# Kernel tuning notes

Measured on AMD Instinct MI355X. Metric: run time of the kernel, lower is better.

Reference implementation:

```python
import jax, jax.numpy as jnp
import numpy as np

HEADS = 8


def setup_inputs() -> dict:
    key = jax.random.key(0)
    ks = jax.random.split(key, 7)
    b, t, e, h = 4, 2048, 128, HEADS
    x = jax.random.normal(ks[0], (b, t, e), dtype=jnp.float32)
    mask = jax.random.randint(ks[1], (1, t, t), 0, 2, dtype=jnp.int32)
    Wq = jax.random.normal(ks[2], (e, e * h), dtype=jnp.float32) / np.sqrt(e)
    Wk = jax.random.normal(ks[3], (e, e * h), dtype=jnp.float32) / np.sqrt(e)
    Wv = jax.random.normal(ks[4], (e, e * h), dtype=jnp.float32) / np.sqrt(e)
    Wu = jax.random.normal(ks[5], (e * h, e), dtype=jnp.float32) / np.sqrt(e * h)
    bu = jax.random.normal(ks[6], (e,), dtype=jnp.float32) * 0.01
    return {"x": x, "mask": mask, "Wq": Wq, "Wk": Wk, "Wv": Wv, "Wu": Wu, "bu": bu}


def reference(x, mask, Wq, Wk, Wv, Wu, bu):
    b, t, e = x.shape
    h = HEADS
    scale = e ** (-0.25)  # original scales q and k each by e**(1/4)
    # project and split heads: (b, t, h, e) -> (b, h, t, e)
    q = (x @ Wq).reshape(b, t, h, e).transpose(0, 2, 1, 3) * scale
    k = (x @ Wk).reshape(b, t, h, e).transpose(0, 2, 1, 3) * scale
    v = (x @ Wv).reshape(b, t, h, e).transpose(0, 2, 1, 3)
    dot = jnp.einsum('bhqe,bhke->bhqk', q, k)  # (b, h, t, t)
    # causal mask: strictly-upper triangle set to -inf (mask_diagonal=False -> offset=1)
    causal = jnp.triu(jnp.ones((t, t), dtype=bool), k=1)
    dot = jnp.where(causal, jnp.float32(-np.inf), dot)
    # external mask: positions where mask == 0 set to -1e9 (broadcast over b*h)
    dot = jnp.where((mask == 0)[:, None, :, :], jnp.float32(-1e9), dot)
    att = jax.nn.softmax(dot, axis=-1)
    out = jnp.einsum('bhqk,bhke->bhqe', att, v)
    out = out.transpose(0, 2, 1, 3).reshape(b, t, h * e)
    return out @ Wu + bu
```

## Files before the change

kernel.cpp:

```cpp
#include <hip/hip_runtime.h>
#include <hip/hip_bf16.h>

typedef unsigned short u16;
typedef unsigned int u32;
typedef __attribute__((ext_vector_type(8))) short bf16x8;
typedef __attribute__((ext_vector_type(4))) float f32x4;
typedef __attribute__((ext_vector_type(8))) unsigned short u16x8;
typedef __attribute__((ext_vector_type(2))) unsigned int u32x2;

#define T_ 2048
#define H_ 8
#define BH_ 32
#define M_ 8192
#define SCALE_QK 0.29730177875068026f

__device__ __forceinline__ u16 f2bf(float f) {
  union { __hip_bfloat16 h; u16 u; } cv; cv.h = __float2bfloat16(f); return cv.u;
}
__device__ __forceinline__ float bf2f(u16 u) {
  union { u16 u; __hip_bfloat16 h; } cv; cv.u = u; return __bfloat162float(cv.h);
}
__device__ __forceinline__ void gload16(const u16* g, u16* l) {
  __builtin_amdgcn_global_load_lds(
      (const __attribute__((address_space(1))) void*)g,
      (__attribute__((address_space(3))) void*)l, 16, 0, 0);
}


__global__ __launch_bounds__(256)
void prep_kernel(const float* __restrict__ x, const float* __restrict__ Wq,
                 const float* __restrict__ Wk, const float* __restrict__ Wv,
                 const float* __restrict__ Wu,
                 u16* __restrict__ xb, u16* __restrict__ WT, u16* __restrict__ WuT)
{
  int i = blockIdx.x * 256 + threadIdx.x;
  if (i < M_ * 128) { xb[i] = f2bf(x[i]); return; }
  int j = i - M_ * 128;
  if (j < 3072 * 128) {
    int n = j >> 7, k = j & 127;
    float w;
    if (n < 1024)      w = Wq[k * 1024 + n] * SCALE_QK;
    else if (n < 2048) w = Wk[k * 1024 + (n - 1024)] * SCALE_QK;
    else               w = Wv[k * 1024 + (n - 2048)];
    WT[j] = f2bf(w);
    return;
  }
  int u = j - 3072 * 128;
  if (u < 128 * 1024) {
    int n = u >> 10, k = u & 1023;
    WuT[u] = f2bf(Wu[k * 128 + n]);
  }
}

__global__ __launch_bounds__(256)
void maskprep_kernel(const int* __restrict__ mask, u32* __restrict__ mbits,
                     u32* __restrict__ deglist, u32* __restrict__ degcount,
                     float* __restrict__ cnt0inv)
{
  int wave = threadIdx.x >> 6, lane = threadIdx.x & 63;
  int q = blockIdx.x * 4 + wave;
  const int* row = mask + (long)q * 2048;
  unsigned long long anyvis = 0ull;
  int cnt1 = 0;
  for (int it = 0; it < 32; ++it) {
    int k = it * 64 + lane;
    unsigned long long bal = __ballot(row[k] != 0);
    if (lane == 0) {
      mbits[q * 64 + it * 2]     = (u32)bal;
      mbits[q * 64 + it * 2 + 1] = (u32)(bal >> 32);
    }
    cnt1 += __popcll(bal);
    int lim = q - it * 64;
    if (lim >= 63)      anyvis |= bal;
    else if (lim >= 0)  anyvis |= (bal & ((2ull << lim) - 1ull));
  }
  if (lane == 0) {
    int c0 = 2048 - cnt1;
    cnt0inv[q] = (c0 > 0) ? 1.0f / (float)c0 : 0.0f;
    if (anyvis == 0ull) {
      u32 slot = atomicAdd(degcount, 1u);
      deglist[slot] = (u32)q;
    }
  }
}

__global__ __launch_bounds__(256)
void qkv_kernel(const u16* __restrict__ xb, const u16* __restrict__ WT,
                u16* __restrict__ Qb, u16* __restrict__ Kimg, u16* __restrict__ Vimg)
{
  __shared__ __align__(16) u16 As[128 * 128];
  __shared__ __align__(16) u16 Bs[128 * 128];
  const int tid = threadIdx.x;
  const int n0 = blockIdx.x * 128;
  const int m0 = blockIdx.y * 128;
#pragma unroll
  for (int i = 0; i < 8; ++i) {
    int c = tid + 256 * i;
    int row = c >> 4, d0 = (c & 15) * 8;
    int soff = row * 128 + ((((d0 >> 3)) ^ (row & 15)) << 3);
    *(u16x8*)(&As[soff]) = *(const u16x8*)(&xb[(m0 + row) * 128 + d0]);
    *(u16x8*)(&Bs[soff]) = *(const u16x8*)(&WT[(n0 + row) * 128 + d0]);
  }
  __syncthreads();
  const int wave = tid >> 6, lane = tid & 63;
  const int lr = lane & 15, lg = lane >> 4;
  const int wm = (wave >> 1) * 64, wn = (wave & 1) * 64;
  f32x4 acc[4][4];
#pragma unroll
  for (int a = 0; a < 4; ++a)
#pragma unroll
    for (int b = 0; b < 4; ++b) acc[a][b] = (f32x4){0.f, 0.f, 0.f, 0.f};
#pragma unroll
  for (int ks = 0; ks < 4; ++ks) {
    bf16x8 af[4], bf[4];
#pragma unroll
    for (int mt = 0; mt < 4; ++mt) {
      int row = wm + mt * 16 + lr, chunk = lg + ks * 4;
      af[mt] = *(const bf16x8*)(&As[row * 128 + ((chunk ^ (row & 15)) << 3)]);
    }
#pragma unroll
    for (int nt = 0; nt < 4; ++nt) {
      int row = wn + nt * 16 + lr, chunk = lg + ks * 4;
      bf[nt] = *(const bf16x8*)(&Bs[row * 128 + ((chunk ^ (row & 15)) << 3)]);
    }
#pragma unroll
    for (int mt = 0; mt < 4; ++mt)
#pragma unroll
      for (int nt = 0; nt < 4; ++nt)
        acc[mt][nt] = __builtin_amdgcn_mfma_f32_16x16x32_bf16(af[mt], bf[nt], acc[mt][nt], 0, 0, 0);
  }
  const int mat = n0 >> 10;
  const int hh = (n0 & 1023) >> 7;
  const int bb = m0 >> 11;
  const long bhb = (long)(bb * H_ + hh);
  __syncthreads();
  if (mat != 2) {
#pragma unroll
    for (int mt = 0; mt < 4; ++mt)
#pragma unroll
      for (int nt = 0; nt < 4; ++nt)
#pragma unroll
        for (int r = 0; r < 4; ++r) {
          int tl = wm + mt * 16 + lg * 4 + r;
          int d  = wn + nt * 16 + lr;
          As[tl * 128 + ((((d >> 3)) ^ (tl & 15)) << 3) + (d & 7)] = f2bf(acc[mt][nt][r]);
        }
    __syncthreads();
    if (mat == 0) {
#pragma unroll
      for (int i = 0; i < 8; ++i) {
        int c = tid + 256 * i;
        int row = c >> 4, d0 = (c & 15) * 8;
        u16x8 v = *(const u16x8*)(&As[row * 128 + ((((d0 >> 3)) ^ (row & 15)) << 3)]);
        *(u16x8*)(&Qb[(bhb * T_ + ((m0 + row) & 2047)) * 128 + d0]) = v;
      }
    } else {
#pragma unroll
      for (int i = 0; i < 8; ++i) {
        int c = tid + 256 * i;
        int row = c >> 4, d0 = (c & 15) * 8;
        u16x8 v = *(const u16x8*)(&As[row * 128 + ((((d0 >> 3)) ^ (row & 15)) << 3)]);
        int t = (m0 + row) & 2047;
        int kt = t >> 6, kr = t & 63;
        *(u16x8*)(&Kimg[(bhb * 32 + kt) * 8192 + kr * 128 + ((((d0 >> 3)) ^ (kr & 15)) << 3)]) = v;
      }
    }
  } else {
    u16* TT = As;
#pragma unroll
    for (int mt = 0; mt < 4; ++mt)
#pragma unroll
      for (int nt = 0; nt < 4; ++nt)
#pragma unroll
        for (int r = 0; r < 4; ++r) {
          int tl = wm + mt * 16 + lg * 4 + r;
          int d  = wn + nt * 16 + lr;
          TT[d * 128 + ((((tl >> 3)) ^ (d & 15)) << 3) + (tl & 7)] = f2bf(acc[mt][nt][r]);
        }
    __syncthreads();
    const int tg0 = m0 & 2047;
#pragma unroll
    for (int i = 0; i < 8; ++i) {
      int c = tid + 256 * i;
      int d = c >> 4, t0 = (c & 15) * 8;
      u16x8 v = *(const u16x8*)(&TT[d * 128 + ((((t0 >> 3)) ^ (d & 15)) << 3)]);
      int tg = tg0 + t0;
      int kt = tg >> 6, kk = tg & 63;
      *(u16x8*)(&Vimg[(bhb * 32 + kt) * 8192 + d * 64 + (((kk >> 3) ^ (d & 7)) << 3)]) = v;
    }
  }
}

__global__ __launch_bounds__(256, 4)
void flash_kernel(const u16* __restrict__ Qb, const u16* __restrict__ Kimg,
                  const u16* __restrict__ Vimg, const u32* __restrict__ mbits,
                  u16* __restrict__ Ob)
{
  __shared__ __align__(16) u16 Ks[64 * 128];
  __shared__ __align__(16) u16 VTs[128 * 64];
  __shared__ __align__(16) u16 Ps[4][16 * 64];
  const int tid = threadIdx.x;
  const int qt = 31 - (blockIdx.x >> 5);
  const int bh = blockIdx.x & 31;
  const int q0 = qt * 64;
  const int wave = tid >> 6, lane = tid & 63;
  const int lr = lane & 15, lg = lane >> 4;
  const long base = (long)bh * T_ * 128;
  const long iblk = (long)bh * 32;
  const int woff = wave * 2048;
  const int qrl = wave * 16 + lr;
  const int swz = (lr & 7) << 1;

  bf16x8 qf[4];
  {
    const u16* qrow = Qb + base + (long)(q0 + qrl) * 128;
#pragma unroll
    for (int ks = 0; ks < 4; ++ks)
      qf[ks] = *(const bf16x8*)(&qrow[lg * 8 + ks * 32]);
  }
  f32x4 acc[8];
#pragma unroll
  for (int i = 0; i < 8; ++i) acc[i] = (f32x4){0.f, 0.f, 0.f, 0.f};
  float mrun = -__builtin_inff(), lrun = 0.f;

  for (int kt = 0; kt <= qt; ++kt) {
    const int kv0 = kt * 64;
    __syncthreads();
    {
      const u16* ks = Kimg + (iblk + kt) * 8192 + woff + lane * 8;
      const u16* vs = Vimg + (iblk + kt) * 8192 + woff + lane * 8;
#pragma unroll
      for (int i = 0; i < 4; ++i) gload16(ks + i * 512, &Ks[woff + i * 512]);
#pragma unroll
      for (int i = 0; i < 4; ++i) gload16(vs + i * 512, &VTs[woff + i * 512]);
    }
    u32 mw0, mw1;
    {
      const u32* mp = &mbits[(q0 + qrl) * 64 + (kv0 >> 5)];
      mw0 = mp[0]; mw1 = mp[1];
    }
    __syncthreads();

    f32x4 s[4];
    __builtin_amdgcn_s_setprio(1);
#pragma unroll
    for (int ft = 0; ft < 4; ++ft) {
      f32x4 sa = (f32x4){0.f, 0.f, 0.f, 0.f};
#pragma unroll
      for (int ks = 0; ks < 4; ++ks) {
        int kr = ft * 16 + lr, chunk = lg + ks * 4;
        bf16x8 kf = *(const bf16x8*)(&Ks[kr * 128 + ((chunk ^ (kr & 15)) << 3)]);
        sa = __builtin_amdgcn_mfma_f32_16x16x32_bf16(kf, qf[ks], sa, 0, 0, 0);
      }
      s[ft] = sa;
    }
    __builtin_amdgcn_s_setprio(0);
    const bool diag = (kt == qt);
#pragma unroll
    for (int ft = 0; ft < 4; ++ft) {
      u32 w = (ft & 2) ? mw1 : mw0;
      int kbase = ft * 16 + lg * 4;
      int sh = ((ft & 1) << 4) + lg * 4;
#pragma unroll
      for (int r = 0; r < 4; ++r) {
        bool vis = (w >> (sh + r)) & 1u;
        if (diag && (kbase + r) > qrl) vis = false;
        if (!vis) s[ft][r] = -__builtin_inff();
      }
    }
    float t0 = fmaxf(fmaxf(s[0][0], s[0][1]), fmaxf(s[0][2], s[0][3]));
    float t1 = fmaxf(fmaxf(s[1][0], s[1][1]), fmaxf(s[1][2], s[1][3]));
    float t2 = fmaxf(fmaxf(s[2][0], s[2][1]), fmaxf(s[2][2], s[2][3]));
    float t3 = fmaxf(fmaxf(s[3][0], s[3][1]), fmaxf(s[3][2], s[3][3]));
    float tm = fmaxf(fmaxf(t0, t1), fmaxf(t2, t3));
    tm = fmaxf(tm, __shfl_xor(tm, 16));
    tm = fmaxf(tm, __shfl_xor(tm, 32));
    float mnew = fmaxf(mrun, tm);
    float msafe = (mnew == -__builtin_inff()) ? 0.f : mnew;
    float fac = __expf(mrun - msafe);
    mrun = mnew;
    float rs = 0.f;
#pragma unroll
    for (int ft = 0; ft < 4; ++ft) {
      float p0 = __expf(s[ft][0] - msafe), p1 = __expf(s[ft][1] - msafe);
      float p2 = __expf(s[ft][2] - msafe), p3 = __expf(s[ft][3] - msafe);
      s[ft][0] = p0; s[ft][1] = p1; s[ft][2] = p2; s[ft][3] = p3;
      rs += (p0 + p1) + (p2 + p3);
    }
    rs += __shfl_xor(rs, 16);
    rs += __shfl_xor(rs, 32);
    lrun = lrun * fac + rs;
#pragma unroll
    for (int nt = 0; nt < 8; ++nt)
#pragma unroll
      for (int r = 0; r < 4; ++r) acc[nt][r] *= fac;
#pragma unroll
    for (int ft = 0; ft < 4; ++ft) {
      u16 h0 = f2bf(s[ft][0]), h1 = f2bf(s[ft][1]);
      u16 h2 = f2bf(s[ft][2]), h3 = f2bf(s[ft][3]);
      u32x2 pw; pw[0] = (u32)h0 | ((u32)h1 << 16); pw[1] = (u32)h2 | ((u32)h3 << 16);
      int ch4 = (ft * 4 + lg) ^ swz;
      *(u32x2*)(&Ps[wave][lr * 64 + ch4 * 4]) = pw;
    }
    bf16x8 pa[2];
#pragma unroll
    for (int s2 = 0; s2 < 2; ++s2) {
      int ch4b = (s2 * 8 + lg * 2) ^ swz;
      pa[s2] = *(const bf16x8*)(&Ps[wave][lr * 64 + ch4b * 4]);
    }
    __builtin_amdgcn_s_setprio(1);
#pragma unroll
    for (int nt = 0; nt < 8; ++nt)
#pragma unroll
      for (int s2 = 0; s2 < 2; ++s2) {
        int d = nt * 16 + lr, chunk = lg + s2 * 4;
        bf16x8 vf = *(const bf16x8*)(&VTs[d * 64 + ((chunk ^ (d & 7)) << 3)]);
        acc[nt] = __builtin_amdgcn_mfma_f32_16x16x32_bf16(vf, pa[s2], acc[nt], 0, 0, 0);
      }
    __builtin_amdgcn_s_setprio(0);
  }
  const float inv = (lrun > 0.f) ? 1.f / lrun : 0.f;
  const long orow = base + (long)(q0 + qrl) * 128;
#pragma unroll
  for (int nt = 0; nt < 8; ++nt) {
    u16 h0 = f2bf(acc[nt][0] * inv), h1 = f2bf(acc[nt][1] * inv);
    u16 h2 = f2bf(acc[nt][2] * inv), h3 = f2bf(acc[nt][3] * inv);
    u32x2 ow; ow[0] = (u32)h0 | ((u32)h1 << 16); ow[1] = (u32)h2 | ((u32)h3 << 16);
    *(u32x2*)(&Ob[orow + nt * 16 + lg * 4]) = ow;
  }
}

__global__ __launch_bounds__(256)
void fixup_partial_kernel(const u32* __restrict__ deglist, const u32* __restrict__ degcount,
                          const u32* __restrict__ mbits, const u16* __restrict__ Vimg,
                          float* __restrict__ partial)
{
  const int slot = blockIdx.z;
  const u32 cnt = *degcount;
  if (slot >= (int)cnt) return;
  const int ksec = blockIdx.x, bh = blockIdx.y;
  const int q = (int)deglist[slot];
  const int t = threadIdx.x;
  const int d = t & 127, kc = t >> 7;
  const u16* vb = Vimg + ((long)bh * 32 + ksec) * 8192 + d * 64;
  const u32 w0 = mbits[q * 64 + ksec * 2];
  const u32 w1 = mbits[q * 64 + ksec * 2 + 1];
  float a = 0.f;
#pragma unroll
  for (int i = 0; i < 4; ++i) {
    int c = kc * 4 + i;
    u32 bits = ((kc == 0) ? (w0 >> (c * 8)) : (w1 >> ((c - 4) * 8))) & 0xffu;
    u16x8 v = *(const u16x8*)(&vb[(c ^ (d & 7)) << 3]);
#pragma unroll
    for (int j = 0; j < 8; ++j)
      a += ((bits >> j) & 1u) ? 0.f : bf2f(v[j]);
  }
  __shared__ float tmp[2][128];
  tmp[kc][d] = a;
  __syncthreads();
  if (t < 128)
    partial[(((long)slot * BH_ + bh) * 128 + d) * 32 + ksec] = tmp[0][d] + tmp[1][d];
}

__global__ __launch_bounds__(128)
void fixup_combine_kernel(const u32* __restrict__ deglist, const u32* __restrict__ degcount,
                          const float* __restrict__ cnt0inv, const float* __restrict__ partial,
                          u16* __restrict__ Ob)
{
  const int slot = blockIdx.x;
  const u32 cnt = *degcount;
  if (slot >= (int)cnt) return;
  const int bh = blockIdx.y;
  const int q = (int)deglist[slot];
  const int d = threadIdx.x;
  const float* p = partial + (((long)slot * BH_ + bh) * 128 + d) * 32;
  float s = 0.f;
#pragma unroll
  for (int i = 0; i < 8; ++i) {
    f32x4 v = *(const f32x4*)(&p[i * 4]);
    s += (v[0] + v[1]) + (v[2] + v[3]);
  }
  Ob[((long)bh * T_ + q) * 128 + d] = f2bf(s * cnt0inv[q]);
}

__global__ __launch_bounds__(256)
void fixup_slow_kernel(const u32* __restrict__ deglist, const u32* __restrict__ degcount,
                       const float* __restrict__ cnt0inv, const u32* __restrict__ mbits,
                       const u16* __restrict__ Vimg, u16* __restrict__ Ob)
{
  const u32 cnt = *degcount;
  const int bh = blockIdx.y;
  const int d = threadIdx.x & 127, half = threadIdx.x >> 7;
  __shared__ float tmp[2][128];
  const u16* vb = Vimg + (long)bh * 32 * 8192;
  for (u32 idx = 8 + blockIdx.x; idx < cnt; idx += gridDim.x) {
    const int q = (int)deglist[idx];
    const float inv = cnt0inv[q];
    float a = 0.f;
#pragma unroll 16
    for (int i = 0; i < 128; ++i) {
      int k0 = half * 1024 + i * 8;
      u32 w = mbits[q * 64 + (k0 >> 5)];
      u32 bits = (w >> (k0 & 31)) & 0xffu;
      int kt = k0 >> 6, kk = k0 & 63;
      u16x8 v = *(const u16x8*)(&vb[(long)kt * 8192 + d * 64 + (((kk >> 3) ^ (d & 7)) << 3)]);
#pragma unroll
      for (int j = 0; j < 8; ++j)
        a += ((bits >> j) & 1u) ? 0.f : bf2f(v[j]);
    }
    tmp[half][d] = a;
    __syncthreads();
    if (half == 0)
      Ob[((long)bh * T_ + q) * 128 + d] = f2bf((tmp[0][d] + tmp[1][d]) * inv);
    __syncthreads();
  }
}

__global__ __launch_bounds__(256)
void outproj_kernel(const u16* __restrict__ Ob, const u16* __restrict__ WuT,
                    const float* __restrict__ bu, float* __restrict__ out)
{
  __shared__ __align__(16) u16 As[32 * 128];
  __shared__ __align__(16) u16 Bs[128 * 128];
  const int tid = threadIdx.x;
  const int m0 = blockIdx.x * 32;
  const int wave = tid >> 6, lane = tid & 63;
  const int lr = lane & 15, lg = lane >> 4;
  f32x4 acc[2][2];
#pragma unroll
  for (int a = 0; a < 2; ++a)
#pragma unroll
    for (int b = 0; b < 2; ++b) acc[a][b] = (f32x4){0.f, 0.f, 0.f, 0.f};
  for (int kc = 0; kc < 8; ++kc) {
    __syncthreads();
#pragma unroll
    for (int i = 0; i < 2; ++i) {
      int c = tid + 256 * i;
      int row = c >> 4, d0 = (c & 15) * 8;
      int m = m0 + row, bb = m >> 11, t = m & 2047;
      *(u16x8*)(&As[row * 128 + ((((d0 >> 3)) ^ (row & 15)) << 3)]) =
          *(const u16x8*)(&Ob[((long)(bb * H_ + kc) * T_ + t) * 128 + d0]);
    }
#pragma unroll
    for (int i = 0; i < 8; ++i) {
      int c = tid + 256 * i;
      int row = c >> 4, d0 = (c & 15) * 8;
      *(u16x8*)(&Bs[row * 128 + ((((d0 >> 3)) ^ (row & 15)) << 3)]) =
          *(const u16x8*)(&WuT[row * 1024 + kc * 128 + d0]);
    }
    __syncthreads();
#pragma unroll
    for (int ks = 0; ks < 4; ++ks) {
      bf16x8 af[2], bf2[2];
#pragma unroll
      for (int mt = 0; mt < 2; ++mt) {
        int row = mt * 16 + lr, chunk = lg + ks * 4;
        af[mt] = *(const bf16x8*)(&As[row * 128 + ((chunk ^ (row & 15)) << 3)]);
      }
#pragma unroll
      for (int nt = 0; nt < 2; ++nt) {
        int row = wave * 32 + nt * 16 + lr, chunk = lg + ks * 4;
        bf2[nt] = *(const bf16x8*)(&Bs[row * 128 + ((chunk ^ (row & 15)) << 3)]);
      }
#pragma unroll
      for (int mt = 0; mt < 2; ++mt)
#pragma unroll
        for (int nt = 0; nt < 2; ++nt)
          acc[mt][nt] = __builtin_amdgcn_mfma_f32_16x16x32_bf16(af[mt], bf2[nt], acc[mt][nt], 0, 0, 0);
    }
  }
#pragma unroll
  for (int mt = 0; mt < 2; ++mt)
#pragma unroll
    for (int nt = 0; nt < 2; ++nt) {
      int n = wave * 32 + nt * 16 + lr;
      float bias = bu[n];
#pragma unroll
      for (int r = 0; r < 4; ++r) {
        int m = m0 + mt * 16 + lg * 4 + r;
        out[(long)m * 128 + n] = acc[mt][nt][r] + bias;
      }
    }
}

extern "C" void kernel_launch(void* const* d_in, const int* in_sizes, int n_in,
                              void* d_out, int out_size, void* d_ws, size_t ws_size,
                              hipStream_t stream)
{
  (void)in_sizes; (void)n_in; (void)out_size; (void)ws_size;
  const float* x   = (const float*)d_in[0];
  const int*   msk = (const int*)d_in[1];
  const float* Wq  = (const float*)d_in[2];
  const float* Wk  = (const float*)d_in[3];
  const float* Wv  = (const float*)d_in[4];
  const float* Wu  = (const float*)d_in[5];
  const float* bu  = (const float*)d_in[6];
  float* out = (float*)d_out;

  u16* Qb   = (u16*)d_ws;
  u16* Kimg = Qb + (size_t)BH_ * T_ * 128;
  u16* Vimg = Kimg + (size_t)BH_ * T_ * 128;
  u16* Obf  = Vimg + (size_t)BH_ * T_ * 128;
  u16* xb   = Obf + (size_t)BH_ * T_ * 128;
  u16* WT   = xb + (size_t)M_ * 128;
  u16* WuT  = WT + (size_t)3072 * 128;
  u32* mbits   = (u32*)(WuT + (size_t)128 * 1024);
  u32* deglist = mbits + (size_t)2048 * 64;
  u32* degcount = deglist + 2048;
  float* cnt0inv = (float*)(degcount + 1);
  float* partial = (float*)Qb;

  hipMemsetAsync(degcount, 0, sizeof(u32), stream);
  prep_kernel<<<6144, 256, 0, stream>>>(x, Wq, Wk, Wv, Wu, xb, WT, WuT);
  maskprep_kernel<<<512, 256, 0, stream>>>(msk, mbits, deglist, degcount, cnt0inv);
  qkv_kernel<<<dim3(24, 64), 256, 0, stream>>>(xb, WT, Qb, Kimg, Vimg);
  flash_kernel<<<1024, 256, 0, stream>>>(Qb, Kimg, Vimg, mbits, Obf);
  fixup_partial_kernel<<<dim3(32, 32, 8), 256, 0, stream>>>(deglist, degcount, mbits, Vimg, partial);
  fixup_combine_kernel<<<dim3(8, 32), 128, 0, stream>>>(deglist, degcount, cnt0inv, partial, Obf);
  fixup_slow_kernel<<<dim3(32, 32), 256, 0, stream>>>(deglist, degcount, cnt0inv, mbits, Vimg, Obf);
  outproj_kernel<<<256, 256, 0, stream>>>(Obf, WuT, bu, out);
}
```

Measured before the change: 140.9 us.

## Register-prefetch next K/V tile and skip rescale when running max unchanged

Replaces direct global-to-LDS loads with a register-staged prefetch. The next K/V tile is loaded into registers while the current tile is computed, then written to LDS at the top of the next iteration, which is meant to hide global load latency. The accumulator rescale is skipped when no lane's running max changed, saving multiplies. Occupancy is lowered from 4 to 3 blocks per SM to make room for the extra prefetch registers, which risks reducing latency hiding across waves.

Measured after the change: 135.8 us. 3.7% less time.

```diff
diff --git a/kernel.cpp b/kernel.cpp
--- a/kernel.cpp
+++ b/kernel.cpp
@@ -19,11 +19,6 @@
 }
 __device__ __forceinline__ float bf2f(u16 u) {
   union { u16 u; __hip_bfloat16 h; } cv; cv.u = u; return __bfloat162float(cv.h);
-}
-__device__ __forceinline__ void gload16(const u16* g, u16* l) {
-  __builtin_amdgcn_global_load_lds(
-      (const __attribute__((address_space(1))) void*)g,
-      (__attribute__((address_space(3))) void*)l, 16, 0, 0);
 }
 
 
@@ -191,7 +186,7 @@
   }
 }
 
-__global__ __launch_bounds__(256, 4)
+__global__ __launch_bounds__(256, 3)
 void flash_kernel(const u16* __restrict__ Qb, const u16* __restrict__ Kimg,
                   const u16* __restrict__ Vimg, const u32* __restrict__ mbits,
                   u16* __restrict__ Ob)
@@ -207,7 +202,7 @@
   const int lr = lane & 15, lg = lane >> 4;
   const long base = (long)bh * T_ * 128;
   const long iblk = (long)bh * 32;
-  const int woff = wave * 2048;
+  const int ldsoff = wave * 2048 + lane * 8;
   const int qrl = wave * 16 + lr;
   const int swz = (lr & 7) << 1;
 
@@ -223,23 +218,39 @@
   for (int i = 0; i < 8; ++i) acc[i] = (f32x4){0.f, 0.f, 0.f, 0.f};
   float mrun = -__builtin_inff(), lrun = 0.f;
 
+  u16x8 kreg[4], vreg[4];
+  {
+    const u16* ks0 = Kimg + iblk * 8192 + ldsoff;
+    const u16* vs0 = Vimg + iblk * 8192 + ldsoff;
+#pragma unroll
+    for (int i = 0; i < 4; ++i) {
+      kreg[i] = *(const u16x8*)(ks0 + i * 512);
+      vreg[i] = *(const u16x8*)(vs0 + i * 512);
+    }
+  }
+
   for (int kt = 0; kt <= qt; ++kt) {
-    const int kv0 = kt * 64;
-    __syncthreads();
-    {
-      const u16* ks = Kimg + (iblk + kt) * 8192 + woff + lane * 8;
-      const u16* vs = Vimg + (iblk + kt) * 8192 + woff + lane * 8;
-#pragma unroll
-      for (int i = 0; i < 4; ++i) gload16(ks + i * 512, &Ks[woff + i * 512]);
-#pragma unroll
-      for (int i = 0; i < 4; ++i) gload16(vs + i * 512, &VTs[woff + i * 512]);
+    __syncthreads();
+#pragma unroll
+    for (int i = 0; i < 4; ++i) {
+      *(u16x8*)(&Ks[ldsoff + i * 512]) = kreg[i];
+      *(u16x8*)(&VTs[ldsoff + i * 512]) = vreg[i];
+    }
+    __syncthreads();
+    if (kt < qt) {
+      const u16* ksn = Kimg + (iblk + kt + 1) * 8192 + ldsoff;
+      const u16* vsn = Vimg + (iblk + kt + 1) * 8192 + ldsoff;
+#pragma unroll
+      for (int i = 0; i < 4; ++i) {
+        kreg[i] = *(const u16x8*)(ksn + i * 512);
+        vreg[i] = *(const u16x8*)(vsn + i * 512);
+      }
     }
     u32 mw0, mw1;
     {
-      const u32* mp = &mbits[(q0 + qrl) * 64 + (kv0 >> 5)];
+      const u32* mp = &mbits[(q0 + qrl) * 64 + kt * 2];
       mw0 = mp[0]; mw1 = mp[1];
     }
-    __syncthreads();
 
     f32x4 s[4];
     __builtin_amdgcn_s_setprio(1);
@@ -278,6 +289,7 @@
     float mnew = fmaxf(mrun, tm);
     float msafe = (mnew == -__builtin_inff()) ? 0.f : mnew;
     float fac = __expf(mrun - msafe);
+    const bool grew = (mnew != mrun);
     mrun = mnew;
     float rs = 0.f;
 #pragma unroll
@@ -290,10 +302,12 @@
     rs += __shfl_xor(rs, 16);
     rs += __shfl_xor(rs, 32);
     lrun = lrun * fac + rs;
-#pragma unroll
-    for (int nt = 0; nt < 8; ++nt)
-#pragma unroll
-      for (int r = 0; r < 4; ++r) acc[nt][r] *= fac;
+    if (__any(grew)) {
+#pragma unroll
+      for (int nt = 0; nt < 8; ++nt)
+#pragma unroll
+        for (int r = 0; r < 4; ++r) acc[nt][r] *= fac;
+    }
 #pragma unroll
     for (int ft = 0; ft < 4; ++ft) {
       u16 h0 = f2bf(s[ft][0]), h1 = f2bf(s[ft][1]);
```
